# Optimization experiments

Measured on AMD Instinct MI355X. Metric: run time of the kernel, lower is better.

The kernel has to match this reference:

```python
import jax, jax.numpy as jnp
import numpy as np

B, T, D = 2, 2048, 2048
HQ, HKV, HD = 16, 8, 128
GROUP = HQ // HKV
EPS = 1e-6


def rms_norm(x, scale):
    # qwen3-compatible: compute in fp32
    xf = x.astype(jnp.float32)
    var = jnp.mean(xf * xf, axis=-1, keepdims=True)
    return (xf * jax.lax.rsqrt(var + EPS) * scale).astype(x.dtype)


def apply_rope(x, cos, sin):
    # x: [B,H,T,d]; cos,sin: [T,d]
    d2 = x.shape[-1] // 2
    x1, x2 = x[..., :d2], x[..., d2:]
    rot = jnp.concatenate([-x2, x1], axis=-1)
    return (x * cos[None, None] + rot * sin[None, None]).astype(x.dtype)


def setup_inputs() -> dict:
    key = jax.random.key(0)
    ks = jax.random.split(key, 8)
    x = jax.random.normal(ks[0], (B, T, D), dtype=jnp.float32)
    # causal mask: True where attention is disallowed (j > i)
    mask = jnp.triu(jnp.ones((T, T), dtype=jnp.bool_), k=1)
    # RoPE tables
    inv_freq = 1.0 / (10000.0 ** (np.arange(0, HD, 2, dtype=np.float32) / HD))
    pos = np.arange(T, dtype=np.float32)
    ang = np.outer(pos, inv_freq)  # [T, HD/2]
    ang = np.concatenate([ang, ang], axis=-1)  # [T, HD]
    cos = jnp.asarray(np.cos(ang), dtype=jnp.float32)
    sin = jnp.asarray(np.sin(ang), dtype=jnp.float32)
    s = 0.02
    Wq = jax.random.normal(ks[1], (HQ * HD, D), dtype=jnp.float32) * s
    Wk = jax.random.normal(ks[2], (HKV * HD, D), dtype=jnp.float32) * s
    Wv = jax.random.normal(ks[3], (HKV * HD, D), dtype=jnp.float32) * s
    Wo = jax.random.normal(ks[4], (D, HQ * HD), dtype=jnp.float32) * s
    q_scale = jnp.ones((HD,), dtype=jnp.float32)
    k_scale = jnp.ones((HD,), dtype=jnp.float32)
    return {"x": x, "mask": mask, "cos": cos, "sin": sin,
            "Wq": Wq, "Wk": Wk, "Wv": Wv, "Wo": Wo,
            "q_scale": q_scale, "k_scale": k_scale}


def reference(x, mask, cos, sin, Wq, Wk, Wv, Wo, q_scale, k_scale):
    Bc, Tc, _ = x.shape
    Q = jnp.einsum('btd,ed->bte', x, Wq).reshape(Bc, Tc, HQ, HD).transpose(0, 2, 1, 3)
    K = jnp.einsum('btd,ed->bte', x, Wk).reshape(Bc, Tc, HKV, HD).transpose(0, 2, 1, 3)
    V = jnp.einsum('btd,ed->bte', x, Wv).reshape(Bc, Tc, HKV, HD).transpose(0, 2, 1, 3)
    Q = rms_norm(Q, q_scale)
    K = rms_norm(K, k_scale)
    Q = apply_rope(Q, cos, sin)
    K = apply_rope(K, cos, sin)
    K = jnp.repeat(K, GROUP, axis=1)  # [B,HQ,T,d]
    V = jnp.repeat(V, GROUP, axis=1)
    S = jnp.einsum('bhqd,bhkd->bhqk', Q, K) / jnp.sqrt(jnp.float32(HD))
    S = jnp.where(mask[None, None], -jnp.inf, S)
    P = jax.nn.softmax(S, axis=-1)
    ctx = jnp.einsum('bhqk,bhkd->bhqd', P, V).transpose(0, 2, 1, 3).reshape(Bc, Tc, HQ * HD)
    return jnp.einsum('bte,de->btd', ctx, Wo)
```

## Files before the change

kernel.cpp:

```cpp
#include <hip/hip_runtime.h>
#include <cstdint>
#include <cstddef>

#define B_ 2
#define T_ 2048
#define D_ 2048
#define HQ_ 16
#define HKV_ 8
#define HD_ 128

typedef __attribute__((ext_vector_type(8))) short short8;
typedef __attribute__((ext_vector_type(8))) unsigned short ushort8;
typedef __attribute__((ext_vector_type(4))) float f32x4;
typedef __attribute__((ext_vector_type(2))) unsigned short ushort2v;
typedef __attribute__((ext_vector_type(4))) unsigned short ushort4v;
typedef __attribute__((ext_vector_type(2))) float float2v;
typedef __attribute__((ext_vector_type(4))) float float4v;

__device__ __forceinline__ unsigned short f2bf(float f) {
  unsigned int u = __builtin_bit_cast(unsigned int, f);
  u += 0x7fffu + ((u >> 16) & 1u);
  return (unsigned short)(u >> 16);
}
__device__ __forceinline__ float bf2f(unsigned short h) {
  unsigned int u = ((unsigned int)h) << 16;
  return __builtin_bit_cast(float, u);
}

#if defined(__has_builtin)
#if __has_builtin(__builtin_amdgcn_global_load_lds)
#define HAS_GLL 1
#endif
#endif
#ifndef HAS_GLL
#define HAS_GLL 0
#endif

__device__ __forceinline__ void gll16(const void* g, void* l) {
#if HAS_GLL
  __builtin_amdgcn_global_load_lds((const __attribute__((address_space(1))) void*)g,
                                   (__attribute__((address_space(3))) void*)l, 16, 0, 0);
#else
  *(ushort8*)((char*)l + (threadIdx.x & 63) * 16) = *(const ushort8*)g;
#endif
}

__global__ __launch_bounds__(256) void cast_all(const float* __restrict__ x,
                                                const float* __restrict__ wq,
                                                const float* __restrict__ wk,
                                                const float* __restrict__ wv,
                                                const float* __restrict__ wo,
                                                unsigned short* __restrict__ xb,
                                                unsigned short* __restrict__ wqkv,
                                                unsigned short* __restrict__ wob) {
  int i = (blockIdx.x * 256 + threadIdx.x) * 4;
  if (i >= 20971520) return;
  const float* s;
  unsigned short* d;
  int soff, doff;
  if (i < 8388608)       { s = x;  soff = i;            d = xb;   doff = i; }
  else if (i < 12582912) { s = wq; soff = i - 8388608;  d = wqkv; doff = i - 8388608; }
  else if (i < 14680064) { s = wk; soff = i - 12582912; d = wqkv; doff = i - 8388608; }
  else if (i < 16777216) { s = wv; soff = i - 14680064; d = wqkv; doff = i - 8388608; }
  else                   { s = wo; soff = i - 16777216; d = wob;  doff = i - 16777216; }
  float4v v = *(const float4v*)(s + soff);
  ushort4v o; o.x = f2bf(v.x); o.y = f2bf(v.y); o.z = f2bf(v.z); o.w = f2bf(v.w);
  *(ushort4v*)(d + doff) = o;
}

#define PH_SYNC { __builtin_amdgcn_s_barrier(); \
                  asm volatile("s_waitcnt lgkmcnt(0)" ::: "memory"); \
                  __builtin_amdgcn_sched_barrier(0); \
                  __builtin_amdgcn_s_setprio(1); }
#define PH_END  { __builtin_amdgcn_s_setprio(0); \
                  __builtin_amdgcn_s_barrier(); \
                  __builtin_amdgcn_sched_barrier(0); }

#define LDA(BUF, QM) { \
  _Pragma("unroll") for (int ii = 0; ii < 4; ii++) { \
    _Pragma("unroll") for (int ks = 0; ks < 2; ks++) \
      a[ii][ks] = *(const short8*)&Abuf[BUF][((QM)*128 + wm*64 + ii*16 + c)*64 + (((ks*4+g)^cs)*8)]; } }

#define LDB(BUF, QN, BB) { \
  _Pragma("unroll") for (int jj = 0; jj < 2; jj++) { \
    _Pragma("unroll") for (int ks = 0; ks < 2; ks++) \
      BB[jj][ks] = *(const short8*)&Bbuf[BUF][((QN)*128 + wn*32 + jj*16 + c)*64 + (((ks*4+g)^cs)*8)]; } }

#define MM(QM, QN, BB) { \
  _Pragma("unroll") for (int ii = 0; ii < 4; ii++) { \
    _Pragma("unroll") for (int jj = 0; jj < 2; jj++) { \
      f32x4 t_ = __builtin_amdgcn_mfma_f32_16x16x32_bf16(a[ii][0], BB[jj][0], acc[(QM)*4+ii][(QN)*2+jj], 0, 0, 0); \
      acc[(QM)*4+ii][(QN)*2+jj] = __builtin_amdgcn_mfma_f32_16x16x32_bf16(a[ii][1], BB[jj][1], t_, 0, 0, 0); } } }

template<int M, int N, int K, bool BF16_OUT>
__global__ __launch_bounds__(512, 2) void gemm8(const unsigned short* __restrict__ A,
                                                const unsigned short* __restrict__ W,
                                                void* __restrict__ Cout) {
  __shared__ __align__(16) unsigned short Abuf[2][256 * 64];
  __shared__ __align__(16) unsigned short Bbuf[2][256 * 64];
  const int tid = threadIdx.x;
  const int lane = tid & 63;
  const int wv = tid >> 6;
  const int g = lane >> 4;
  const int c = lane & 15;
  const int cs = c & 7;
  const int wm = wv >> 2;
  const int wn = wv & 3;

  constexpr int NT = N / 256;
  constexpr int NWG = (M / 256) * NT;
  constexpr int CHUNK = NWG / 8;
  const int bid = blockIdx.x;
  const int swz = (bid & 7) * CHUNK + (bid >> 3);
  const int m0 = (swz / NT) * 256;
  const int n0 = (swz % NT) * 256;

  const int prl = wv * 8 + (lane >> 3);
  const int scl = lane & 7;
#define STA(BUF, P0, KO) { \
    int pr_ = (P0) + prl; \
    int lr_ = ((pr_ >> 6) & 1) * 128 + ((pr_ >> 7) & 1) * 64 + (pr_ & 63); \
    int lc_ = (scl ^ (pr_ & 7)) * 8; \
    gll16(&A[(size_t)(m0 + lr_) * K + (KO) + lc_], &Abuf[BUF][(P0) * 64 + wv * 512]); }
#define STB(BUF, P0, KO) { \
    int pr_ = (P0) + prl; \
    int lr_ = ((pr_ >> 5) & 3) * 64 + ((pr_ >> 7) & 1) * 32 + (pr_ & 31); \
    int lc_ = (scl ^ (pr_ & 7)) * 8; \
    gll16(&W[(size_t)(n0 + lr_) * K + (KO) + lc_], &Bbuf[BUF][(P0) * 64 + wv * 512]); }

  short8 a[4][2], b0[2][2], b1[2][2];
  f32x4 acc[8][4];
#pragma unroll
  for (int i = 0; i < 8; i++)
#pragma unroll
    for (int j = 0; j < 4; j++) acc[i][j] = (f32x4)0.0f;

  STA(0, 0, 0); STA(0, 64, 0); STA(0, 128, 0); STA(0, 192, 0);
  STB(0, 0, 0); STB(0, 64, 0); STB(0, 128, 0); STB(0, 192, 0);
  STA(1, 0, 64); STA(1, 64, 64); STA(1, 128, 64); STA(1, 192, 64);
  STB(1, 0, 64); STB(1, 64, 64); STB(1, 128, 64); STB(1, 192, 64);
  asm volatile("s_waitcnt vmcnt(8)" ::: "memory");
  __builtin_amdgcn_s_barrier();

  constexpr int NITER = K / 128;
  for (int it = 0; it < NITER - 1; ++it) {
    const int k2 = it * 128 + 128;
    const int k3 = k2 + 64;
    LDA(0, 0); LDB(0, 0, b0);
    PH_SYNC; MM(0, 0, b0); PH_END;
    LDB(0, 1, b1);
    STA(0, 0, k2); STA(0, 64, k2); STB(0, 0, k2); STB(0, 64, k2);
    PH_SYNC; MM(0, 1, b1); PH_END;
    LDA(0, 1);
    STB(0, 128, k2); STB(0, 192, k2);
    PH_SYNC; MM(1, 1, b1); PH_END;
    STA(0, 128, k2); STA(0, 192, k2);
    asm volatile("s_waitcnt vmcnt(8)" ::: "memory");
    PH_SYNC; MM(1, 0, b0); PH_END;
    LDA(1, 0); LDB(1, 0, b0);
    PH_SYNC; MM(0, 0, b0); PH_END;
    LDB(1, 1, b1);
    STA(1, 0, k3); STA(1, 64, k3); STB(1, 0, k3); STB(1, 64, k3);
    PH_SYNC; MM(0, 1, b1); PH_END;
    LDA(1, 1);
    STB(1, 128, k3); STB(1, 192, k3);
    PH_SYNC; MM(1, 1, b1); PH_END;
    STA(1, 128, k3); STA(1, 192, k3);
    asm volatile("s_waitcnt vmcnt(8)" ::: "memory");
    PH_SYNC; MM(1, 0, b0); PH_END;
  }
  LDA(0, 0); LDB(0, 0, b0); PH_SYNC; MM(0, 0, b0); PH_END;
  LDB(0, 1, b1);            PH_SYNC; MM(0, 1, b1); PH_END;
  LDA(0, 1);                PH_SYNC; MM(1, 1, b1); PH_END;
  asm volatile("s_waitcnt vmcnt(0)" ::: "memory");
  PH_SYNC; MM(1, 0, b0); PH_END;
  LDA(1, 0); LDB(1, 0, b0); PH_SYNC; MM(0, 0, b0); PH_END;
  LDB(1, 1, b1);            PH_SYNC; MM(0, 1, b1); PH_END;
  LDA(1, 1);                PH_SYNC; MM(1, 1, b1); PH_END;
  PH_SYNC; MM(1, 0, b0); PH_END;

#pragma unroll
  for (int I = 0; I < 8; I++)
#pragma unroll
    for (int J = 0; J < 4; J++)
#pragma unroll
      for (int r = 0; r < 4; r++) {
        int row = m0 + wm * 128 + I * 16 + g * 4 + r;
        int col = n0 + wn * 64 + J * 16 + c;
        if (BF16_OUT)
          ((unsigned short*)Cout)[(size_t)row * N + col] = f2bf(acc[I][J][r]);
        else
          ((float*)Cout)[(size_t)row * N + col] = acc[I][J][r];
      }
#undef STA
#undef STB
}

__global__ __launch_bounds__(256) void qk_norm_rope(const unsigned short* __restrict__ qkv,
                                                    const float* __restrict__ cosT,
                                                    const float* __restrict__ sinT,
                                                    const float* __restrict__ q_scale,
                                                    const float* __restrict__ k_scale,
                                                    unsigned short* __restrict__ Qb,
                                                    unsigned short* __restrict__ Kb) {
  const int tid = threadIdx.x;
  const int lane = tid & 63;
  const int wv = tid >> 6;
  const int row = blockIdx.x;
  const int b = row >> 11;
  const int t = row & 2047;
  const int d0 = lane * 2;

  const float2v cs = *(const float2v*)&cosT[t * 128 + d0];
  const float2v sn = *(const float2v*)&sinT[t * 128 + d0];
  const float2v qsc = *(const float2v*)&q_scale[d0];
  const float2v ksc = *(const float2v*)&k_scale[d0];
  const float sgn = (lane < 32) ? -1.0f : 1.0f;
  const unsigned short* base = qkv + (size_t)row * 4096;

#pragma unroll
  for (int s6 = 0; s6 < 6; s6++) {
    const int slot = wv * 6 + s6;
    const bool isQ = slot < 16;
    const unsigned short* src = base + (isQ ? slot * 128 : 2048 + (slot - 16) * 128);
    ushort2v u = *(const ushort2v*)&src[d0];
    float x0 = bf2f(u.x), x1 = bf2f(u.y);
    float ss = x0 * x0 + x1 * x1;
    ss += __shfl_xor(ss, 1);  ss += __shfl_xor(ss, 2);  ss += __shfl_xor(ss, 4);
    ss += __shfl_xor(ss, 8);  ss += __shfl_xor(ss, 16); ss += __shfl_xor(ss, 32);
    float rinv = rsqrtf(ss * (1.0f / 128.0f) + 1e-6f);
    float2v scv = isQ ? qsc : ksc;
    float xn0 = x0 * rinv * scv.x;
    float xn1 = x1 * rinv * scv.y;
    float o0 = __shfl_xor(xn0, 32);
    float o1 = __shfl_xor(xn1, 32);
    float r0v = xn0 * cs.x + sgn * o0 * sn.x;
    float r1v = xn1 * cs.y + sgn * o1 * sn.y;
    ushort2v out; out.x = f2bf(r0v); out.y = f2bf(r1v);
    unsigned short* dst;
    if (isQ) dst = Qb + ((size_t)(b * HQ_ + slot) * T_ + t) * HD_;
    else     dst = Kb + ((size_t)(b * HKV_ + (slot - 16)) * T_ + t) * HD_;
    *(ushort2v*)&dst[d0] = out;
  }
}

__global__ __launch_bounds__(256) void v_transpose(const unsigned short* __restrict__ qkv,
                                                   unsigned short* __restrict__ Vt) {
  __shared__ unsigned short lds[128 * 65];
  const int tid = threadIdx.x;
  const int blk = blockIdx.x;
  const int tblk = blk & 31;
  const int kv = (blk >> 5) & 7;
  const int b = blk >> 8;
  const int t0 = tblk * 64;
  const int r = tid >> 2;
  const int seg = tid & 3;
  const unsigned short* src = qkv + (size_t)(b * T_ + t0 + r) * 4096 + 3072 + kv * 128;
  for (int i = 0; i < 4; i++) {
    int cc = seg * 32 + i * 8;
    ushort8 v = *(const ushort8*)&src[cc];
    for (int q = 0; q < 8; q++) lds[(cc + q) * 65 + r] = v[q];
  }
  __syncthreads();
  const int cI = tid >> 1;
  const int rs = (tid & 1) * 32;
  unsigned short* dst = Vt + ((size_t)(b * HKV_ + kv) * HD_ + cI) * T_ + t0 + rs;
  const unsigned short* srow = &lds[cI * 65 + rs];
  for (int j = 0; j < 32; j += 4) {
    ushort4v v; v.x = srow[j]; v.y = srow[j + 1]; v.z = srow[j + 2]; v.w = srow[j + 3];
    *(ushort4v*)&dst[j] = v;
  }
}

__global__ __launch_bounds__(256) void attn(const unsigned short* __restrict__ Qb,
                                            const unsigned short* __restrict__ Kb,
                                            const unsigned short* __restrict__ Vt,
                                            unsigned short* __restrict__ ctxb) {
  __shared__ __align__(16) unsigned short Ks[64 * 128];
  __shared__ __align__(16) unsigned short Vs[128 * 64];
  __shared__ __align__(16) unsigned short Ps[4][16 * 72];
  const int tid = threadIdx.x;
  const int lane = tid & 63;
  const int wv = tid >> 6;
  const int g = lane >> 4;
  const int c = lane & 15;

  const int blk = blockIdx.x;
  const int kv = blk & 7;
  const int idx = blk >> 3;
  const int p = idx >> 2;
  const int b = (idx >> 1) & 1;
  const int h = kv * 2 + (idx & 1);

  const unsigned short* Kh = Kb + (size_t)(b * HKV_ + kv) * T_ * HD_;
  const unsigned short* Vh = Vt + (size_t)(b * HKV_ + kv) * HD_ * T_;
  const float scale = 0.08838834764831845f;

  for (int ph = 0; ph < 2; ph++) {
    const int qb = ph ? (31 - p) : p;
    const int nkt = qb + 1;
    const unsigned short* Qh = Qb + ((size_t)(b * HQ_ + h) * T_ + qb * 64 + wv * 16) * HD_;

    short8 aq[4];
#pragma unroll
    for (int dk = 0; dk < 4; dk++) aq[dk] = *(const short8*)&Qh[c * HD_ + dk * 32 + g * 8];

    f32x4 acc[8];
#pragma unroll
    for (int dc = 0; dc < 8; dc++) acc[dc] = (f32x4)0.0f;
    float lp[4] = {0.0f, 0.0f, 0.0f, 0.0f};

    for (int kt = 0; kt < nkt; kt++) {
      __syncthreads();
#pragma unroll
      for (int i = 0; i < 4; i++) {
        const int ch = wv * 256 + i * 64 + lane;
        const int rowK = ch >> 4, ccK = ch & 15;
        const int sK = ccK ^ (rowK & 7);
        gll16(Kh + (size_t)(kt * 64 + rowK) * HD_ + sK * 8,
              Ks + (size_t)(wv * 256 + i * 64) * 8);
        const int rowV = ch >> 3, ccV = ch & 7;
        const int sV = ccV ^ (rowV & 7);
        gll16(Vh + (size_t)rowV * T_ + kt * 64 + sV * 8,
              Vs + (size_t)(wv * 256 + i * 64) * 8);
      }
      __syncthreads();

      f32x4 s[4];
#pragma unroll
      for (int kf = 0; kf < 4; kf++) s[kf] = (f32x4)0.0f;
#pragma unroll
      for (int dk = 0; dk < 4; dk++) {
#pragma unroll
        for (int kf = 0; kf < 4; kf++) {
          short8 bk = *(const short8*)&Ks[(kf * 16 + c) * 128 + ((dk * 4 + g) ^ (c & 7)) * 8];
          s[kf] = __builtin_amdgcn_mfma_f32_16x16x32_bf16(aq[dk], bk, s[kf], 0, 0, 0);
        }
      }

      const bool diag = (kt == nkt - 1);
#pragma unroll
      for (int kf = 0; kf < 4; kf++) {
#pragma unroll
        for (int r = 0; r < 4; r++) {
          float pv = __expf(s[kf][r] * scale);
          if (diag) {
            int key = kt * 64 + kf * 16 + c;
            int rowq = qb * 64 + wv * 16 + g * 4 + r;
            if (key > rowq) pv = 0.0f;
          }
          lp[r] += pv;
          Ps[wv][(g * 4 + r) * 72 + kf * 16 + c] = f2bf(pv);
        }
      }

      short8 ap[2];
      ap[0] = *(const short8*)&Ps[wv][c * 72 + g * 8];
      ap[1] = *(const short8*)&Ps[wv][c * 72 + 32 + g * 8];
#pragma unroll
      for (int dc = 0; dc < 8; dc++) {
#pragma unroll
        for (int kf2 = 0; kf2 < 2; kf2++) {
          short8 bv = *(const short8*)&Vs[(dc * 16 + c) * 64 + ((kf2 * 4 + g) ^ (c & 7)) * 8];
          acc[dc] = __builtin_amdgcn_mfma_f32_16x16x32_bf16(ap[kf2], bv, acc[dc], 0, 0, 0);
        }
      }
    }

#pragma unroll
    for (int r = 0; r < 4; r++) {
      float l = lp[r];
      l += __shfl_xor(l, 1); l += __shfl_xor(l, 2);
      l += __shfl_xor(l, 4); l += __shfl_xor(l, 8);
      float inv = 1.0f / l;
      int row = b * T_ + qb * 64 + wv * 16 + g * 4 + r;
#pragma unroll
      for (int dc = 0; dc < 8; dc++)
        ctxb[(size_t)row * (HQ_ * HD_) + h * HD_ + dc * 16 + c] = f2bf(acc[dc][r] * inv);
    }
  }
}

extern "C" void kernel_launch(void* const* d_in, const int* in_sizes, int n_in,
                              void* d_out, int out_size, void* d_ws, size_t ws_size,
                              hipStream_t stream) {
  const float* x = (const float*)d_in[0];
  const float* cosT = (const float*)d_in[2];
  const float* sinT = (const float*)d_in[3];
  const float* Wq = (const float*)d_in[4];
  const float* Wk = (const float*)d_in[5];
  const float* Wv = (const float*)d_in[6];
  const float* Wo = (const float*)d_in[7];
  const float* q_scale = (const float*)d_in[8];
  const float* k_scale = (const float*)d_in[9];

  char* ws = (char*)d_ws;
  unsigned short* qkv  = (unsigned short*)(ws + 0);
  unsigned short* ctxb = qkv;
  unsigned short* xb   = (unsigned short*)(ws + 33554432);
  unsigned short* wqkv = (unsigned short*)(ws + 50331648);
  unsigned short* wob  = (unsigned short*)(ws + 67108864);
  unsigned short* Qb   = (unsigned short*)(ws + 75497472);
  unsigned short* Kb   = (unsigned short*)(ws + 92274688);
  unsigned short* Vt   = (unsigned short*)(ws + 100663296);

  cast_all<<<20480, 256, 0, stream>>>(x, Wq, Wk, Wv, Wo, xb, wqkv, wob);
  gemm8<4096, 4096, 2048, true><<<256, 512, 0, stream>>>(xb, wqkv, qkv);
  qk_norm_rope<<<4096, 256, 0, stream>>>(qkv, cosT, sinT, q_scale, k_scale, Qb, Kb);
  v_transpose<<<512, 256, 0, stream>>>(qkv, Vt);
  attn<<<512, 256, 0, stream>>>(Qb, Kb, Vt, ctxb);
  gemm8<4096, 2048, 2048, false><<<128, 512, 0, stream>>>(ctxb, wob, d_out);
}
```

Baseline: 357.2 us.

## Double-buffer K/V tiles in attention and raise MFMA wave priority

```diff
diff --git a/kernel.cpp b/kernel.cpp
--- a/kernel.cpp
+++ b/kernel.cpp
@@ -276,8 +276,8 @@
                                             const unsigned short* __restrict__ Kb,
                                             const unsigned short* __restrict__ Vt,
                                             unsigned short* __restrict__ ctxb) {
-  __shared__ __align__(16) unsigned short Ks[64 * 128];
-  __shared__ __align__(16) unsigned short Vs[128 * 64];
+  __shared__ __align__(16) unsigned short Ks[2][64 * 128];
+  __shared__ __align__(16) unsigned short Vs[2][128 * 64];
   __shared__ __align__(16) unsigned short Ps[4][16 * 72];
   const int tid = threadIdx.x;
   const int lane = tid & 63;
@@ -296,6 +296,16 @@
   const unsigned short* Vh = Vt + (size_t)(b * HKV_ + kv) * HD_ * T_;
   const float scale = 0.08838834764831845f;
 
+#define STAGE_KV(BF, KT) { \
+  _Pragma("unroll") for (int i_ = 0; i_ < 4; i_++) { \
+    const int ch_ = wv * 256 + i_ * 64 + lane; \
+    const int rK_ = ch_ >> 4, cK_ = ch_ & 15; \
+    gll16(Kh + (size_t)((KT) * 64 + rK_) * HD_ + (cK_ ^ (rK_ & 7)) * 8, \
+          Ks[BF] + (size_t)(wv * 256 + i_ * 64) * 8); \
+    const int rV_ = ch_ >> 3, cV_ = ch_ & 7; \
+    gll16(Vh + (size_t)rV_ * T_ + (KT) * 64 + (cV_ ^ (rV_ & 7)) * 8, \
+          Vs[BF] + (size_t)(wv * 256 + i_ * 64) * 8); } }
+
   for (int ph = 0; ph < 2; ph++) {
     const int qb = ph ? (31 - p) : p;
     const int nkt = qb + 1;
@@ -310,33 +320,27 @@
     for (int dc = 0; dc < 8; dc++) acc[dc] = (f32x4)0.0f;
     float lp[4] = {0.0f, 0.0f, 0.0f, 0.0f};
 
+    STAGE_KV(0, 0);
+    __syncthreads();
+
     for (int kt = 0; kt < nkt; kt++) {
-      __syncthreads();
-#pragma unroll
-      for (int i = 0; i < 4; i++) {
-        const int ch = wv * 256 + i * 64 + lane;
-        const int rowK = ch >> 4, ccK = ch & 15;
-        const int sK = ccK ^ (rowK & 7);
-        gll16(Kh + (size_t)(kt * 64 + rowK) * HD_ + sK * 8,
-              Ks + (size_t)(wv * 256 + i * 64) * 8);
-        const int rowV = ch >> 3, ccV = ch & 7;
-        const int sV = ccV ^ (rowV & 7);
-        gll16(Vh + (size_t)rowV * T_ + kt * 64 + sV * 8,
-              Vs + (size_t)(wv * 256 + i * 64) * 8);
-      }
-      __syncthreads();
+      const int cur = kt & 1;
+      if (kt + 1 < nkt) { STAGE_KV(cur ^ 1, kt + 1); }
+      __builtin_amdgcn_sched_barrier(0);
 
       f32x4 s[4];
 #pragma unroll
       for (int kf = 0; kf < 4; kf++) s[kf] = (f32x4)0.0f;
+      __builtin_amdgcn_s_setprio(1);
 #pragma unroll
       for (int dk = 0; dk < 4; dk++) {
 #pragma unroll
         for (int kf = 0; kf < 4; kf++) {
-          short8 bk = *(const short8*)&Ks[(kf * 16 + c) * 128 + ((dk * 4 + g) ^ (c & 7)) * 8];
+          short8 bk = *(const short8*)&Ks[cur][(kf * 16 + c) * 128 + ((dk * 4 + g) ^ (c & 7)) * 8];
           s[kf] = __builtin_amdgcn_mfma_f32_16x16x32_bf16(aq[dk], bk, s[kf], 0, 0, 0);
         }
       }
+      __builtin_amdgcn_s_setprio(0);
 
       const bool diag = (kt == nkt - 1);
 #pragma unroll
@@ -357,14 +361,18 @@
       short8 ap[2];
       ap[0] = *(const short8*)&Ps[wv][c * 72 + g * 8];
       ap[1] = *(const short8*)&Ps[wv][c * 72 + 32 + g * 8];
+      __builtin_amdgcn_s_setprio(1);
 #pragma unroll
       for (int dc = 0; dc < 8; dc++) {
 #pragma unroll
         for (int kf2 = 0; kf2 < 2; kf2++) {
-          short8 bv = *(const short8*)&Vs[(dc * 16 + c) * 64 + ((kf2 * 4 + g) ^ (c & 7)) * 8];
+          short8 bv = *(const short8*)&Vs[cur][(dc * 16 + c) * 64 + ((kf2 * 4 + g) ^ (c & 7)) * 8];
           acc[dc] = __builtin_amdgcn_mfma_f32_16x16x32_bf16(ap[kf2], bv, acc[dc], 0, 0, 0);
         }
       }
+      __builtin_amdgcn_s_setprio(0);
+
+      __syncthreads();
     }
 
 #pragma unroll
@@ -379,6 +387,7 @@
         ctxb[(size_t)row * (HQ_ * HD_) + h * HD_ + dc * 16 + c] = f2bf(acc[dc][r] * inv);
     }
   }
+#undef STAGE_KV
 }
 
 extern "C" void kernel_launch(void* const* d_in, const int* in_sizes, int n_in,
```

After: 346.9 us. -2.9%, faster.
